# Kernel tuning notes

Hardware: AMD Instinct MI355X
Metric: run time of the kernel (lower is better)

Reference implementation:

```python
import jax, jax.numpy as jnp
import numpy as np

DIM, HEAD, SR = 512, 8, 2
LN_EPS = 1e-5


def _layernorm(x, g, b):
    mu = jnp.mean(x, axis=-1, keepdims=True)
    var = jnp.mean((x - mu) ** 2, axis=-1, keepdims=True)
    return (x - mu) * jax.lax.rsqrt(var + LN_EPS) * g + b


def setup_inputs() -> dict:
    key = jax.random.key(0)
    ks = jax.random.split(key, 16)
    B, N, C = 8, 4096, DIM
    s = 1.0 / np.sqrt(C)
    inp = {
        "x": jax.random.normal(ks[0], (B, N, C), jnp.float32),
        "context": jax.random.normal(ks[1], (B, N, C), jnp.float32),
        # Linear weights in torch layout [out, in]
        "Wq": jax.random.normal(ks[2], (C, C), jnp.float32) * s,
        "bq": jnp.zeros((C,), jnp.float32),
        "Wk": jax.random.normal(ks[3], (C, C), jnp.float32) * s,
        "bk": jnp.zeros((C,), jnp.float32),
        "Wv": jax.random.normal(ks[4], (C, C), jnp.float32) * s,
        "bv": jnp.zeros((C,), jnp.float32),
        "Wp": jax.random.normal(ks[5], (C, C), jnp.float32) * s,
        "bp": jnp.zeros((C,), jnp.float32),
        # spatial-reduction convs, OIHW, kernel=stride=SR
        "Wsrk": jax.random.normal(ks[6], (C, C, SR, SR), jnp.float32) * s / SR,
        "bsrk": jnp.zeros((C,), jnp.float32),
        "Wsrv": jax.random.normal(ks[7], (C, C, SR, SR), jnp.float32) * s / SR,
        "bsrv": jnp.zeros((C,), jnp.float32),
        "gk": jnp.ones((C,), jnp.float32),
        "bek": jnp.zeros((C,), jnp.float32),
        "gv": jnp.ones((C,), jnp.float32),
        "bev": jnp.zeros((C,), jnp.float32),
        "H": 64,
        "W": 64,
    }
    return inp


def reference(x, context, Wq, bq, Wk, bk, Wv, bv, Wp, bp,
              Wsrk, bsrk, Wsrv, bsrv, gk, bek, gv, bev, H, W):
    B, N, C = x.shape
    h, d = HEAD, C // HEAD
    scale = d ** (-0.5)

    # spatial reduction on context (sr_ratio > 1 branch)
    ctx = jnp.transpose(context, (0, 2, 1)).reshape(B, C, H, W)  # [B,C,H,W]
    dn = (("NCHW", "OIHW", "NCHW"))

    def sr(kernel, bias):
        y = jax.lax.conv_general_dilated(ctx, kernel, (SR, SR), "VALID",
                                         dimension_numbers=dn)
        y = y + bias[None, :, None, None]
        return jnp.transpose(y.reshape(B, C, -1), (0, 2, 1))  # [B,M,C]

    ctx_k = _layernorm(sr(Wsrk, bsrk), gk, bek)
    ctx_v = _layernorm(sr(Wsrv, bsrv), gv, bev)

    q = (x @ Wq.T + bq).reshape(B, N, h, d)          # [B,N,h,d]
    k = (ctx_k @ Wk.T + bk).reshape(B, -1, h, d)     # [B,M,h,d]
    v = (ctx_v @ Wv.T + bv).reshape(B, -1, h, d)     # [B,M,h,d]

    attn = jnp.einsum("bnhd,bmhd->bhnm", q, k) * scale
    attn = jax.nn.softmax(attn, axis=-1)
    out = jnp.einsum("bhnm,bmhd->bnhd", attn, v).reshape(B, N, C)
    return out @ Wp.T + bp
```

## Files before the change

### kernel.cpp

```cpp
#include <hip/hip_runtime.h>
#include <hip/hip_bf16.h>

typedef float f32x4 __attribute__((ext_vector_type(4)));
typedef short bf16x8 __attribute__((ext_vector_type(8)));
typedef unsigned short ushort_t;

__device__ __forceinline__ ushort_t f2bf(float f) {
    union { float f; unsigned u; } v; v.f = f;
    unsigned r = v.u + 0x7fffu + ((v.u >> 16) & 1u);
    return (ushort_t)(r >> 16);
}
__device__ __forceinline__ float bf2f(ushort_t h) {
    union { unsigned u; float f; } v; v.u = ((unsigned)h) << 16;
    return v.f;
}

__device__ __forceinline__ void async16(ushort_t* lds, const ushort_t* g) {
    __builtin_amdgcn_global_load_lds(
        (const __attribute__((address_space(1))) unsigned int*)g,
        (__attribute__((address_space(3))) unsigned int*)lds, 16, 0, 0);
}

__global__ __launch_bounds__(256) void cast_bf16_kernel(const float* __restrict__ src,
                                                        ushort_t* __restrict__ dst, long n) {
    long i = ((long)blockIdx.x * 256 + threadIdx.x) * 8;
    if (i >= n) return;
    float4 a = *(const float4*)(src + i);
    float4 b = *(const float4*)(src + i + 4);
    ushort_t o[8];
    o[0]=f2bf(a.x); o[1]=f2bf(a.y); o[2]=f2bf(a.z); o[3]=f2bf(a.w);
    o[4]=f2bf(b.x); o[5]=f2bf(b.y); o[6]=f2bf(b.z); o[7]=f2bf(b.w);
    *(bf16x8*)(dst + i) = *(bf16x8*)o;
}

__global__ __launch_bounds__(256) void cast_w4_kernel(const float* __restrict__ s0,
                                                      const float* __restrict__ s1,
                                                      const float* __restrict__ s2,
                                                      const float* __restrict__ s3,
                                                      ushort_t* __restrict__ dst) {
    long idx = (long)blockIdx.x * 256 + threadIdx.x;
    int sel = (int)(idx >> 15);
    const float* s = sel == 0 ? s0 : sel == 1 ? s1 : sel == 2 ? s2 : s3;
    long off = (idx & 32767) * 8;
    float4 a = *(const float4*)(s + off);
    float4 b = *(const float4*)(s + off + 4);
    ushort_t o[8];
    o[0]=f2bf(a.x); o[1]=f2bf(a.y); o[2]=f2bf(a.z); o[3]=f2bf(a.w);
    o[4]=f2bf(b.x); o[5]=f2bf(b.y); o[6]=f2bf(b.z); o[7]=f2bf(b.w);
    *(bf16x8*)(dst + (long)sel * 262144 + off) = *(bf16x8*)o;
}

__global__ __launch_bounds__(256) void pack_wsr2_kernel(const float* __restrict__ w0,
                                                        const float* __restrict__ w1,
                                                        ushort_t* __restrict__ out) {
    int idx = blockIdx.x * 256 + threadIdx.x;
    int sel = idx >> 18;
    const float* w = sel ? w1 : w0;
    int li = idx & 262143;
    int c = li >> 9, ci = li & 511;
    float4 t = *(const float4*)(w + c * 2048 + ci * 4);
    ushort_t* ob = out + sel * 1048576 + c * 2048 + ci;
    ob[0]    = f2bf(t.x);
    ob[512]  = f2bf(t.y);
    ob[1024] = f2bf(t.z);
    ob[1536] = f2bf(t.w);
}

struct GemmJob {
    const ushort_t* A;
    const ushort_t* Bw;
    const float* bias;
    void* C;
    int omode;
    int M;
    int K;
    int gather;
};

__global__ __launch_bounds__(256) void gemm_multi(GemmJob j0, GemmJob j1, GemmJob j2,
                                                  int nb0, int nb1) {
    __shared__ __align__(16) ushort_t As[128][64];
    __shared__ __align__(16) ushort_t Bs[128][64];
    const int bid = blockIdx.x;
    GemmJob j;
    int local;
    if (bid < nb0)            { j = j0; local = bid; }
    else if (bid < nb0 + nb1) { j = j1; local = bid - nb0; }
    else                      { j = j2; local = bid - nb0 - nb1; }

    const int tid  = threadIdx.x;
    const int row0 = (local >> 2) * 128, col0 = (local & 3) * 128;
    const int wave = tid >> 6, lane = tid & 63;
    const int rw = wave >> 1, cw = wave & 1;
    const int l15 = lane & 15, l4 = lane >> 4;
    const int srow = wave * 8 + (lane >> 3);
    const int sc8  = (lane & 7) * 8;
    const int K = j.K;

    f32x4 acc[4][4] = {};

    for (int k0 = 0; k0 < K; k0 += 64) {
        __syncthreads();
#pragma unroll
        for (int p = 0; p < 4; ++p) {
            int r = p * 32 + srow;
            const ushort_t* ga;
            if (j.gather) {
                int gr = row0 + r;
                int b = gr >> 10, m = gr & 1023;
                int mh = m >> 5, mw = m & 31;
                int tap = k0 >> 9;
                int kh = tap >> 1, kw = tap & 1;
                ga = j.A + ((long)(b * 4096 + (2 * mh + kh) * 64 + (2 * mw + kw))) * 512
                         + (k0 & 511) + sc8;
            } else {
                ga = j.A + (long)(row0 + r) * K + k0 + sc8;
            }
            async16(&As[p * 32 + wave * 8][0], ga);
            async16(&Bs[p * 32 + wave * 8][0],
                    j.Bw + (long)(col0 + r) * K + k0 + sc8);
        }
        __syncthreads();
#pragma unroll
        for (int ks = 0; ks < 2; ++ks) {
            bf16x8 af[4], bfr[4];
#pragma unroll
            for (int i = 0; i < 4; ++i)
                af[i] = *(const bf16x8*)&As[rw * 64 + i * 16 + l15][ks * 32 + l4 * 8];
#pragma unroll
            for (int jj = 0; jj < 4; ++jj)
                bfr[jj] = *(const bf16x8*)&Bs[cw * 64 + jj * 16 + l15][ks * 32 + l4 * 8];
#pragma unroll
            for (int i = 0; i < 4; ++i)
#pragma unroll
                for (int jj = 0; jj < 4; ++jj)
                    acc[i][jj] = __builtin_amdgcn_mfma_f32_16x16x32_bf16(af[i], bfr[jj],
                                                                         acc[i][jj], 0, 0, 0);
        }
    }
#pragma unroll
    for (int i = 0; i < 4; ++i) {
#pragma unroll
        for (int jj = 0; jj < 4; ++jj) {
            int col = col0 + cw * 64 + jj * 16 + l15;
            float bv = j.bias[col];
#pragma unroll
            for (int r = 0; r < 4; ++r) {
                int row = row0 + rw * 64 + i * 16 + l4 * 4 + r;
                float v = acc[i][jj][r] + bv;
                if (j.omode == 0) {
                    ((ushort_t*)j.C)[(long)row * 512 + col] = f2bf(v);
                } else if (j.omode == 1) {
                    ((float*)j.C)[(long)row * 512 + col] = v;
                } else {
                    int b = row >> 10, m = row & 1023;
                    int hh = col >> 6, dd = col & 63;
                    ((ushort_t*)j.C)[(((long)(b * 8 + hh) * 64 + dd) << 10) + m] = f2bf(v);
                }
            }
        }
    }
}

__global__ __launch_bounds__(256) void ln_kernel(ushort_t* __restrict__ data,
                                                 const float* __restrict__ g0,
                                                 const float* __restrict__ be0,
                                                 const float* __restrict__ g1,
                                                 const float* __restrict__ be1) {
    int wave = threadIdx.x >> 6, lane = threadIdx.x & 63;
    long row = (long)blockIdx.x * 4 + wave;
    const float* g  = row < 8192 ? g0 : g1;
    const float* be = row < 8192 ? be0 : be1;
    ushort_t* p = data + row * 512 + lane * 8;
    bf16x8 raw = *(bf16x8*)p;
    ushort_t* rp = (ushort_t*)&raw;
    float v[8], s = 0.f, s2 = 0.f;
#pragma unroll
    for (int j = 0; j < 8; ++j) { v[j] = bf2f(rp[j]); s += v[j]; s2 += v[j] * v[j]; }
#pragma unroll
    for (int d = 1; d < 64; d <<= 1) { s += __shfl_xor(s, d); s2 += __shfl_xor(s2, d); }
    float mu  = s * (1.f / 512.f);
    float var = s2 * (1.f / 512.f) - mu * mu;
    float rs  = rsqrtf(var + 1e-5f);
    ushort_t o[8];
#pragma unroll
    for (int j = 0; j < 8; ++j) {
        int c = lane * 8 + j;
        o[j] = f2bf((v[j] - mu) * rs * g[c] + be[c]);
    }
    *(bf16x8*)p = *(bf16x8*)o;
}

__global__ __launch_bounds__(256, 3) void attn_kernel(const ushort_t* __restrict__ q,
                                                      const ushort_t* __restrict__ k,
                                                      const ushort_t* __restrict__ vt,
                                                      ushort_t* __restrict__ o) {
    __shared__ __align__(16) ushort_t Ks[128][72];
    __shared__ __align__(16) ushort_t Vs[64][136];

    const int tid = threadIdx.x;
    const int wave = tid >> 6, lane = tid & 63;
    const int l15 = lane & 15, l4 = lane >> 4;
    const int n0 = blockIdx.x * 128;
    const int hh = blockIdx.y;
    const int b  = blockIdx.z;

    bf16x8 bq[2][2];
#pragma unroll
    for (int nb = 0; nb < 2; ++nb)
#pragma unroll
        for (int ks = 0; ks < 2; ++ks)
            bq[nb][ks] = *(const bf16x8*)(
                q + (long)(b * 4096 + n0 + wave * 32 + nb * 16 + l15) * 512
                  + hh * 64 + ks * 32 + l4 * 8);

    f32x4 oacc[2][4] = {};
    f32x4 lacc[2] = {};
    union { bf16x8 v8; unsigned u[4]; } ones;
    ones.u[0] = ones.u[1] = ones.u[2] = ones.u[3] = 0x3F803F80u;
    const float EC = 0.18033688011112042f;

    for (int c = 0; c < 8; ++c) {
        const int m0 = c * 128;
        __syncthreads();
#pragma unroll
        for (int p = 0; p < 4; ++p) {
            int qi = p * 256 + tid;
            int r = qi >> 3, c8 = (qi & 7) * 8;
            bf16x8 v = *(const bf16x8*)(k + (((long)(b * 1024 + m0 + r) * 8 + hh) << 6) + c8);
            *(bf16x8*)&Ks[r][c8] = v;
        }
#pragma unroll
        for (int p = 0; p < 4; ++p) {
            int qi = p * 256 + tid;
            int dd = qi >> 4, c8 = (qi & 15) * 8;
            bf16x8 v = *(const bf16x8*)(vt + (((long)(b * 8 + hh) * 64 + dd) << 10) + m0 + c8);
            *(bf16x8*)&Vs[dd][c8] = v;
        }
        __syncthreads();

        f32x4 s[2][8] = {};
        __builtin_amdgcn_s_setprio(1);
#pragma unroll
        for (int ks = 0; ks < 2; ++ks) {
#pragma unroll
            for (int i = 0; i < 8; ++i) {
                bf16x8 ak = *(const bf16x8*)&Ks[i * 16 + l15][ks * 32 + l4 * 8];
                s[0][i] = __builtin_amdgcn_mfma_f32_16x16x32_bf16(ak, bq[0][ks], s[0][i], 0, 0, 0);
                s[1][i] = __builtin_amdgcn_mfma_f32_16x16x32_bf16(ak, bq[1][ks], s[1][i], 0, 0, 0);
            }
        }
        __builtin_amdgcn_s_setprio(0);

        unsigned pk[2][8][2];
#pragma unroll
        for (int nb = 0; nb < 2; ++nb)
#pragma unroll
            for (int i = 0; i < 8; ++i) {
                float e0 = __builtin_amdgcn_exp2f(s[nb][i][0] * EC);
                float e1 = __builtin_amdgcn_exp2f(s[nb][i][1] * EC);
                float e2 = __builtin_amdgcn_exp2f(s[nb][i][2] * EC);
                float e3 = __builtin_amdgcn_exp2f(s[nb][i][3] * EC);
                asm("v_cvt_pk_bf16_f32 %0, %1, %2" : "=v"(pk[nb][i][0]) : "v"(e0), "v"(e1));
                asm("v_cvt_pk_bf16_f32 %0, %1, %2" : "=v"(pk[nb][i][1]) : "v"(e2), "v"(e3));
            }

        __builtin_amdgcn_s_setprio(1);
#pragma unroll
        for (int mb = 0; mb < 4; ++mb) {
            union { bf16x8 v8; unsigned long long h[2]; } bfr[4];
#pragma unroll
            for (int db = 0; db < 4; ++db) {
                bfr[db].h[0] = *(const unsigned long long*)&Vs[db * 16 + l15][mb * 32 + l4 * 4];
                bfr[db].h[1] = *(const unsigned long long*)&Vs[db * 16 + l15][mb * 32 + 16 + l4 * 4];
            }
#pragma unroll
            for (int nb = 0; nb < 2; ++nb) {
                union { bf16x8 v8; unsigned u32v[4]; } af;
                af.u32v[0] = pk[nb][2 * mb][0];
                af.u32v[1] = pk[nb][2 * mb][1];
                af.u32v[2] = pk[nb][2 * mb + 1][0];
                af.u32v[3] = pk[nb][2 * mb + 1][1];
                lacc[nb] = __builtin_amdgcn_mfma_f32_16x16x32_bf16(af.v8, ones.v8,
                                                                   lacc[nb], 0, 0, 0);
#pragma unroll
                for (int db = 0; db < 4; ++db)
                    oacc[nb][db] = __builtin_amdgcn_mfma_f32_16x16x32_bf16(af.v8, bfr[db].v8,
                                                                           oacc[nb][db], 0, 0, 0);
            }
        }
        __builtin_amdgcn_s_setprio(0);
    }

#pragma unroll
    for (int nb = 0; nb < 2; ++nb)
#pragma unroll
        for (int r = 0; r < 4; ++r) {
            float inv = 1.f / lacc[nb][r];
            int n = wave * 32 + nb * 16 + l4 * 4 + r;
#pragma unroll
            for (int db = 0; db < 4; ++db) {
                int dd = db * 16 + l15;
                o[((long)(b * 4096 + n0 + n)) * 512 + hh * 64 + dd] = f2bf(oacc[nb][db][r] * inv);
            }
        }
}

extern "C" void kernel_launch(void* const* d_in, const int* in_sizes, int n_in,
                              void* d_out, int out_size, void* d_ws, size_t ws_size,
                              hipStream_t stream) {
    const float* x    = (const float*)d_in[0];
    const float* ctx  = (const float*)d_in[1];
    const float* Wq   = (const float*)d_in[2];
    const float* bq   = (const float*)d_in[3];
    const float* Wk   = (const float*)d_in[4];
    const float* bk   = (const float*)d_in[5];
    const float* Wv   = (const float*)d_in[6];
    const float* bv   = (const float*)d_in[7];
    const float* Wp   = (const float*)d_in[8];
    const float* bp   = (const float*)d_in[9];
    const float* Wsrk = (const float*)d_in[10];
    const float* bsrk = (const float*)d_in[11];
    const float* Wsrv = (const float*)d_in[12];
    const float* bsrv = (const float*)d_in[13];
    const float* gk   = (const float*)d_in[14];
    const float* bek  = (const float*)d_in[15];
    const float* gv   = (const float*)d_in[16];
    const float* bev  = (const float*)d_in[17];

    ushort_t* x_bf    = (ushort_t*)d_ws;
    ushort_t* ctx_bf  = x_bf    + 16777216;
    ushort_t* q_bf    = ctx_bf  + 16777216;
    ushort_t* at_bf   = q_bf    + 16777216;
    ushort_t* k_bf    = at_bf   + 16777216;
    ushort_t* vt_bf   = k_bf    + 4194304;
    ushort_t* convk   = vt_bf   + 4194304;
    ushort_t* convv   = convk   + 4194304;
    ushort_t* wq_bf   = convv   + 4194304;
    ushort_t* wk_bf   = wq_bf   + 262144;
    ushort_t* wv_bf   = wk_bf   + 262144;
    ushort_t* wp_bf   = wv_bf   + 262144;
    ushort_t* wsrk_p  = wp_bf   + 262144;
    ushort_t* wsrv_p  = wsrk_p  + 1048576;

    cast_bf16_kernel<<<8192, 256, 0, stream>>>(x,   x_bf,   16777216);
    cast_bf16_kernel<<<8192, 256, 0, stream>>>(ctx, ctx_bf, 16777216);
    cast_w4_kernel<<<512, 256, 0, stream>>>(Wq, Wk, Wv, Wp, wq_bf);
    pack_wsr2_kernel<<<2048, 256, 0, stream>>>(Wsrk, Wsrv, wsrk_p);

    GemmJob jck = { ctx_bf, wsrk_p, bsrk, convk, 0, 8192,  2048, 1 };
    GemmJob jcv = { ctx_bf, wsrv_p, bsrv, convv, 0, 8192,  2048, 1 };
    GemmJob jq  = { x_bf,  wq_bf,  bq,   q_bf,  0, 32768, 512,  0 };
    gemm_multi<<<1536, 256, 0, stream>>>(jck, jcv, jq, 256, 256);

    ln_kernel<<<4096, 256, 0, stream>>>(convk, gk, bek, gv, bev);

    GemmJob jk  = { convk, wk_bf, bk, k_bf,  0, 8192, 512, 0 };
    GemmJob jv  = { convv, wv_bf, bv, vt_bf, 2, 8192, 512, 0 };
    gemm_multi<<<512, 256, 0, stream>>>(jk, jv, jv, 256, 256);

    attn_kernel<<<dim3(32, 8, 8), 256, 0, stream>>>(q_bf, k_bf, vt_bf, at_bf);

    GemmJob jo  = { at_bf, wp_bf, bp, d_out, 1, 32768, 512, 0 };
    gemm_multi<<<1024, 256, 0, stream>>>(jo, jo, jo, 1024, 0);
}
```

Measured before the change: 454.2 us.

## Merge input casts, fold softmax scale into Q projection, swizzle GEMM tiles

Replaces the two separate fp32-to-bf16 cast launches for x and context with one combined launch. Folds the softmax scale times log2(e) into the Q projection epilogue through a new per-job oscale field, so the attention kernel no longer multiplies each score before exp2. Changes the GEMM block-to-tile mapping so groups of 8 consecutive blocks cover neighbouring rows across the four column tiles, aiming for better L2 reuse of the A rows. Rounding Q to bf16 after scaling slightly changes numerics.

```diff
diff --git a/kernel.cpp b/kernel.cpp
--- a/kernel.cpp
+++ b/kernel.cpp
@@ -21,16 +21,19 @@
         (__attribute__((address_space(3))) unsigned int*)lds, 16, 0, 0);
 }
 
-__global__ __launch_bounds__(256) void cast_bf16_kernel(const float* __restrict__ src,
-                                                        ushort_t* __restrict__ dst, long n) {
-    long i = ((long)blockIdx.x * 256 + threadIdx.x) * 8;
-    if (i >= n) return;
-    float4 a = *(const float4*)(src + i);
-    float4 b = *(const float4*)(src + i + 4);
+__global__ __launch_bounds__(256) void cast2_bf16_kernel(const float* __restrict__ s0,
+                                                         const float* __restrict__ s1,
+                                                         ushort_t* __restrict__ dst) {
+    long idx = (long)blockIdx.x * 256 + threadIdx.x;
+    int sel = (int)(idx >> 21);
+    const float* s = sel ? s1 : s0;
+    long off = (idx & 2097151) * 8;
+    float4 a = *(const float4*)(s + off);
+    float4 b = *(const float4*)(s + off + 4);
     ushort_t o[8];
     o[0]=f2bf(a.x); o[1]=f2bf(a.y); o[2]=f2bf(a.z); o[3]=f2bf(a.w);
     o[4]=f2bf(b.x); o[5]=f2bf(b.y); o[6]=f2bf(b.z); o[7]=f2bf(b.w);
-    *(bf16x8*)(dst + i) = *(bf16x8*)o;
+    *(bf16x8*)(dst + (long)sel * 16777216 + off) = *(bf16x8*)o;
 }
 
 __global__ __launch_bounds__(256) void cast_w4_kernel(const float* __restrict__ s0,
@@ -75,6 +78,7 @@
     int M;
     int K;
     int gather;
+    float oscale;
 };
 
 __global__ __launch_bounds__(256) void gemm_multi(GemmJob j0, GemmJob j1, GemmJob j2,
@@ -89,7 +93,8 @@
     else                      { j = j2; local = bid - nb0 - nb1; }
 
     const int tid  = threadIdx.x;
-    const int row0 = (local >> 2) * 128, col0 = (local & 3) * 128;
+    const int row0 = (((local & 7) | ((local >> 5) << 3))) * 128;
+    const int col0 = ((local >> 3) & 3) * 128;
     const int wave = tid >> 6, lane = tid & 63;
     const int rw = wave >> 1, cw = wave & 1;
     const int l15 = lane & 15, l4 = lane >> 4;
@@ -147,7 +152,7 @@
 #pragma unroll
             for (int r = 0; r < 4; ++r) {
                 int row = row0 + rw * 64 + i * 16 + l4 * 4 + r;
-                float v = acc[i][jj][r] + bv;
+                float v = (acc[i][jj][r] + bv) * j.oscale;
                 if (j.omode == 0) {
                     ((ushort_t*)j.C)[(long)row * 512 + col] = f2bf(v);
                 } else if (j.omode == 1) {
@@ -218,7 +223,6 @@
     f32x4 lacc[2] = {};
     union { bf16x8 v8; unsigned u[4]; } ones;
     ones.u[0] = ones.u[1] = ones.u[2] = ones.u[3] = 0x3F803F80u;
-    const float EC = 0.18033688011112042f;
 
     for (int c = 0; c < 8; ++c) {
         const int m0 = c * 128;
@@ -257,10 +261,10 @@
         for (int nb = 0; nb < 2; ++nb)
 #pragma unroll
             for (int i = 0; i < 8; ++i) {
-                float e0 = __builtin_amdgcn_exp2f(s[nb][i][0] * EC);
-                float e1 = __builtin_amdgcn_exp2f(s[nb][i][1] * EC);
-                float e2 = __builtin_amdgcn_exp2f(s[nb][i][2] * EC);
-                float e3 = __builtin_amdgcn_exp2f(s[nb][i][3] * EC);
+                float e0 = __builtin_amdgcn_exp2f(s[nb][i][0]);
+                float e1 = __builtin_amdgcn_exp2f(s[nb][i][1]);
+                float e2 = __builtin_amdgcn_exp2f(s[nb][i][2]);
+                float e3 = __builtin_amdgcn_exp2f(s[nb][i][3]);
                 asm("v_cvt_pk_bf16_f32 %0, %1, %2" : "=v"(pk[nb][i][0]) : "v"(e0), "v"(e1));
                 asm("v_cvt_pk_bf16_f32 %0, %1, %2" : "=v"(pk[nb][i][1]) : "v"(e2), "v"(e3));
             }
@@ -343,24 +347,25 @@
     ushort_t* wsrk_p  = wp_bf   + 262144;
     ushort_t* wsrv_p  = wsrk_p  + 1048576;
 
-    cast_bf16_kernel<<<8192, 256, 0, stream>>>(x,   x_bf,   16777216);
-    cast_bf16_kernel<<<8192, 256, 0, stream>>>(ctx, ctx_bf, 16777216);
+    const float EC = 0.18033688011112042f;
+
+    cast2_bf16_kernel<<<16384, 256, 0, stream>>>(x, ctx, x_bf);
     cast_w4_kernel<<<512, 256, 0, stream>>>(Wq, Wk, Wv, Wp, wq_bf);
     pack_wsr2_kernel<<<2048, 256, 0, stream>>>(Wsrk, Wsrv, wsrk_p);
 
-    GemmJob jck = { ctx_bf, wsrk_p, bsrk, convk, 0, 8192,  2048, 1 };
-    GemmJob jcv = { ctx_bf, wsrv_p, bsrv, convv, 0, 8192,  2048, 1 };
-    GemmJob jq  = { x_bf,  wq_bf,  bq,   q_bf,  0, 32768, 512,  0 };
+    GemmJob jck = { ctx_bf, wsrk_p, bsrk, convk, 0, 8192,  2048, 1, 1.0f };
+    GemmJob jcv = { ctx_bf, wsrv_p, bsrv, convv, 0, 8192,  2048, 1, 1.0f };
+    GemmJob jq  = { x_bf,  wq_bf,  bq,   q_bf,  0, 32768, 512,  0, EC };
     gemm_multi<<<1536, 256, 0, stream>>>(jck, jcv, jq, 256, 256);
 
     ln_kernel<<<4096, 256, 0, stream>>>(convk, gk, bek, gv, bev);
 
-    GemmJob jk  = { convk, wk_bf, bk, k_bf,  0, 8192, 512, 0 };
-    GemmJob jv  = { convv, wv_bf, bv, vt_bf, 2, 8192, 512, 0 };
+    GemmJob jk  = { convk, wk_bf, bk, k_bf,  0, 8192, 512, 0, 1.0f };
+    GemmJob jv  = { convv, wv_bf, bv, vt_bf, 2, 8192, 512, 0, 1.0f };
     gemm_multi<<<512, 256, 0, stream>>>(jk, jv, jv, 256, 256);
 
     attn_kernel<<<dim3(32, 8, 8), 256, 0, stream>>>(q_bf, k_bf, vt_bf, at_bf);
 
-    GemmJob jo  = { at_bf, wp_bf, bp, d_out, 1, 32768, 512, 0 };
+    GemmJob jo  = { at_bf, wp_bf, bp, d_out, 1, 32768, 512, 0, 1.0f };
     gemm_multi<<<1024, 256, 0, stream>>>(jo, jo, jo, 1024, 0);
 }
```

Measured after the change: 435.3 us. 1.04x faster.
